# Performance work log

Measured on AMD Instinct MI355X. Metric: run time of the kernel, lower is better.

## Reference

```python
import jax, jax.numpy as jnp
import numpy as np

L = 2        # n_layers
IN = 172     # in_channels
HID = 128    # hidden_channels
NH = 4       # heads
HD = HID // NH  # per-head dim = 32
TD = 100     # time_dim
V = 400000   # global node table size
N = 150000   # sampled subgraph nodes
E = 500000   # edges per layer
B = 15000    # seed batch size


def setup_inputs() -> dict:
    key = jax.random.key(0)
    ks = jax.random.split(key, 24)
    p = lambda k, shp, s=0.05: jax.random.normal(k, shp, jnp.float32) * s
    inp = {
        "x_all": jax.random.normal(ks[0], (V, IN), jnp.float32),
        "all_node_ids": jax.random.randint(ks[1], (N,), 0, V),
        "edge_src": jax.random.randint(ks[2], (L, E), 0, N),
        "edge_dst": jax.random.randint(ks[3], (L, E), 0, N),
        "dts": jax.random.uniform(ks[4], (L, E), jnp.float32, 0.0, 1e4),
        "batch_size": B,
        # TimeEncode params
        "basis_freq": jnp.asarray(1.0 / 10 ** np.linspace(0, 9, TD), jnp.float32),
        "phase": jnp.zeros((TD,), jnp.float32),
        # input projection
        "Wp": p(ks[5], (IN, HID)), "bp": jnp.zeros((HID,), jnp.float32),
        # per-layer TransformerConv params (stacked over L)
        "Wq": p(ks[6], (L, HID, HID)), "bq": jnp.zeros((L, HID), jnp.float32),
        "Wk": p(ks[7], (L, HID, HID)), "bk": jnp.zeros((L, HID), jnp.float32),
        "Wv": p(ks[8], (L, HID, HID)), "bv": jnp.zeros((L, HID), jnp.float32),
        "We": p(ks[9], (L, TD, HID)),  # lin_edge, bias=False in PyG
        "Wskip": p(ks[10], (L, HID, HID)), "bskip": jnp.zeros((L, HID), jnp.float32),
        "bn_g": jnp.ones((L, HID), jnp.float32), "bn_b": jnp.zeros((L, HID), jnp.float32),
        # classifier head
        "W1": p(ks[11], (HID, HID)), "b1": jnp.zeros((HID,), jnp.float32),
        "g1": jnp.ones((HID,), jnp.float32), "be1": jnp.zeros((HID,), jnp.float32),
        "W2": p(ks[12], (HID, HID // 2)), "b2": jnp.zeros((HID // 2,), jnp.float32),
        "g2": jnp.ones((HID // 2,), jnp.float32), "be2": jnp.zeros((HID // 2,), jnp.float32),
        "W3": p(ks[13], (HID // 2, 1)), "b3": jnp.zeros((1,), jnp.float32),
    }
    return inp


def _bn(x, g, b):
    # BatchNorm1d, training-mode batch statistics (biased variance), eps=1e-5
    m = x.mean(0)
    v = x.var(0)
    return g * (x - m) * jax.lax.rsqrt(v + 1e-5) + b


def reference(x_all, all_node_ids, edge_src, edge_dst, dts, batch_size,
              basis_freq, phase, Wp, bp, Wq, bq, Wk, bk, Wv, bv, We,
              Wskip, bskip, bn_g, bn_b, W1, b1, g1, be1, W2, b2, g2, be2, W3, b3):
    n = all_node_ids.shape[0]
    x = x_all[all_node_ids]                      # [N, IN] gather from global table
    h = jax.nn.relu(x @ Wp + bp)                 # [N, HID]
    inv_sqrt_d = 1.0 / np.sqrt(HD)
    for i in range(L):
        src, dst, dt = edge_src[i], edge_dst[i], dts[i]
        # learnable sinusoidal time encoding of edge delta-t  [E, TD]
        te = jnp.cos(dt[:, None] * basis_freq[None, :] + phase[None, :])
        q = (h @ Wq[i] + bq[i]).reshape(n, NH, HD)
        k = (h @ Wk[i] + bk[i]).reshape(n, NH, HD)
        v = (h @ Wv[i] + bv[i]).reshape(n, NH, HD)
        e = (te @ We[i]).reshape(-1, NH, HD)     # [E, NH, HD]
        kj = k[src] + e                          # key + edge proj (PyG TransformerConv)
        vj = v[src] + e                          # value + edge proj
        alpha = jnp.einsum('ehd,ehd->eh', q[dst], kj) * inv_sqrt_d  # [E, NH]
        # scatter-softmax over edges grouped by destination node
        m = jax.ops.segment_max(alpha, dst, num_segments=n)
        a = jnp.exp(alpha - m[dst])
        s = jax.ops.segment_sum(a, dst, num_segments=n) + 1e-16
        w = a / s[dst]                           # [E, NH]
        agg = jax.ops.segment_sum(w[:, :, None] * vj, dst, num_segments=n)
        out = agg.reshape(n, HID) + h @ Wskip[i] + bskip[i]  # concat heads + root skip
        h = _bn(jax.nn.relu(out), bn_g[i], bn_b[i])          # dropout = identity (eval)
    hb = h[:batch_size]
    z = jax.nn.relu(_bn(hb @ W1 + b1, g1, be1))
    z = jax.nn.relu(_bn(z @ W2 + b2, g2, be2))
    return (z @ W3 + b3)[:, 0]                   # [batch_size]
```

## Files before the change

kernel.cpp:

```cpp
#include <hip/hip_runtime.h>
#include <hip/hip_bf16.h>
#include <math.h>

#define IN_DIM 172
#define HID 128
#define TDIM 100
#define KPAD 192

typedef __attribute__((ext_vector_type(8))) short bf16x8;
typedef __attribute__((ext_vector_type(4))) float f32x4;

static __device__ __forceinline__ ushort f2b(float x) {
  unsigned u = __float_as_uint(x);
  u += 0x7FFFu + ((u >> 16) & 1u);
  return (ushort)(u >> 16);
}
static __device__ __forceinline__ float blo(unsigned w) { return __uint_as_float(w << 16); }
static __device__ __forceinline__ float bhi(unsigned w) { return __uint_as_float(w & 0xffff0000u); }
static __device__ __forceinline__ float b2f(ushort v) { return __uint_as_float((unsigned)v << 16); }

__global__ void k_prep(const float* __restrict__ Wp,
                       const float* __restrict__ Wq, const float* __restrict__ Wk,
                       const float* __restrict__ Wv, const float* __restrict__ Ws,
                       const float* __restrict__ bq, const float* __restrict__ bk,
                       const float* __restrict__ bv, const float* __restrict__ bs,
                       const float* __restrict__ We, const float* __restrict__ W1,
                       ushort* __restrict__ wpt,
                       ushort* __restrict__ wallT0, ushort* __restrict__ wallT1,
                       float* __restrict__ ball0, float* __restrict__ ball1,
                       ushort* __restrict__ wet0, ushort* __restrict__ wet1,
                       ushort* __restrict__ w1t) {
  int i = blockIdx.x * 256 + threadIdx.x;
  if (i < 128 * KPAD) {
    int c = i / KPAD, k = i - c * KPAD;
    wpt[i] = (k < IN_DIM) ? f2b(Wp[k * HID + c]) : (ushort)0;
    return;
  }
  i -= 128 * KPAD;
  if (i < 2 * 512 * 128) {
    int layer = i >> 16;
    int j = i & 65535;
    int col = j >> 7, k = j & 127;
    int m = col >> 7, c = col & 127;
    const float* W = (m == 0) ? Wq : (m == 1) ? Wk : (m == 2) ? Wv : Ws;
    W += (size_t)layer * HID * HID;
    (layer ? wallT1 : wallT0)[j] = f2b(W[k * HID + c]);
    if (k == 0) {
      const float* bb = (m == 0) ? bq : (m == 1) ? bk : (m == 2) ? bv : bs;
      (layer ? ball1 : ball0)[col] = bb[layer * HID + c];
    }
    return;
  }
  i -= 2 * 512 * 128;
  if (i < 2 * 128 * 128) {
    int layer = i >> 14;
    int j = i & 16383;
    int c = j >> 7, t = j & 127;
    (layer ? wet1 : wet0)[j] =
        (t < TDIM) ? f2b(We[((size_t)layer * TDIM + t) * HID + c]) : (ushort)0;
    return;
  }
  i -= 2 * 128 * 128;
  if (i < 128 * 128) {
    int c = i >> 7, k = i & 127;
    w1t[i] = f2b(W1[k * HID + c]);
  }
}

__global__ __launch_bounds__(256) void k_in_mfma(
    const float* __restrict__ x_all, const int* __restrict__ ids,
    const ushort* __restrict__ wpt, const float* __restrict__ bp,
    ushort* __restrict__ h, int n) {
  __shared__ __align__(16) ushort xs[64][200];
  int tid = threadIdx.x;
  long r0 = (long)blockIdx.x * 64;
  for (int i = tid; i < 64 * 28; i += 256) {
    int r = i / 28, c = IN_DIM + (i - r * 28);
    xs[r][c] = 0;
  }
  for (int i = tid; i < 64 * 43; i += 256) {
    int r = i / 43, seg = i - r * 43;
    long row = r0 + r;
    float4 v = make_float4(0.f, 0.f, 0.f, 0.f);
    if (row < n) v = *(const float4*)(x_all + (size_t)ids[row] * IN_DIM + seg * 4);
    ushort4 u;
    u.x = f2b(v.x); u.y = f2b(v.y); u.z = f2b(v.z); u.w = f2b(v.w);
    *(ushort4*)&xs[r][seg * 4] = u;
  }
  __syncthreads();
  int wv = tid >> 6, l = tid & 63;
  int arow = wv * 16 + (l & 15);
  int kb0 = (l >> 4) * 8;
  bf16x8 a[6];
  #pragma unroll
  for (int kk = 0; kk < 6; ++kk) a[kk] = *(const bf16x8*)&xs[arow][kk * 32 + kb0];
  #pragma unroll
  for (int nt = 0; nt < 8; ++nt) {
    int col = nt * 16 + (l & 15);
    const ushort* wcol = wpt + (size_t)col * KPAD + kb0;
    f32x4 acc = {0.f, 0.f, 0.f, 0.f};
    #pragma unroll
    for (int kk = 0; kk < 6; ++kk) {
      bf16x8 bfr = *(const bf16x8*)(wcol + kk * 32);
      acc = __builtin_amdgcn_mfma_f32_16x16x32_bf16(a[kk], bfr, acc, 0, 0, 0);
    }
    float bias = bp[col];
    #pragma unroll
    for (int j = 0; j < 4; ++j) {
      long row = r0 + wv * 16 + (l >> 4) * 4 + j;
      if (row < n) {
        float y = acc[j] + bias;
        h[row * HID + col] = f2b(y > 0.f ? y : 0.f);
      }
    }
  }
}

template <bool BN_IN>
__global__ __launch_bounds__(512) void k_qkvs(
    const ushort* __restrict__ hbf, const ushort* __restrict__ xf,
    const float* __restrict__ sums, const float* __restrict__ bng,
    const float* __restrict__ bnb, float inv_n,
    const ushort* __restrict__ wallT, const float* __restrict__ ball,
    ushort* __restrict__ qb, ushort* __restrict__ kvb,
    ushort* __restrict__ ob, int n) {
  __shared__ __align__(16) ushort hs[128][136];
  __shared__ float As[128], Bs[128];
  int tid = threadIdx.x;
  if (BN_IN) {
    if (tid < 128) {
      float mean = sums[tid] * inv_n;
      float var = sums[128 + tid] * inv_n - mean * mean;
      float A = bng[tid] * rsqrtf(var + 1e-5f);
      As[tid] = A;
      Bs[tid] = bnb[tid] - mean * A;
    }
    __syncthreads();
  }
  long r0 = (long)blockIdx.x * 128;
  for (int i = tid; i < 128 * 16; i += 512) {
    int r = i >> 4, cseg = i & 15;
    long row = r0 + r;
    int c0 = cseg * 8;
    if (BN_IN) {
      ushort4 ua = {0, 0, 0, 0}, ub = {0, 0, 0, 0};
      if (row < n) {
        uint4 xw = *(const uint4*)(xf + row * HID + c0);
        float x0 = blo(xw.x), x1 = bhi(xw.x), x2 = blo(xw.y), x3 = bhi(xw.y);
        float x4 = blo(xw.z), x5 = bhi(xw.z), x6 = blo(xw.w), x7 = bhi(xw.w);
        ua.x = f2b(As[c0 + 0] * fmaxf(x0, 0.f) + Bs[c0 + 0]);
        ua.y = f2b(As[c0 + 1] * fmaxf(x1, 0.f) + Bs[c0 + 1]);
        ua.z = f2b(As[c0 + 2] * fmaxf(x2, 0.f) + Bs[c0 + 2]);
        ua.w = f2b(As[c0 + 3] * fmaxf(x3, 0.f) + Bs[c0 + 3]);
        ub.x = f2b(As[c0 + 4] * fmaxf(x4, 0.f) + Bs[c0 + 4]);
        ub.y = f2b(As[c0 + 5] * fmaxf(x5, 0.f) + Bs[c0 + 5]);
        ub.z = f2b(As[c0 + 6] * fmaxf(x6, 0.f) + Bs[c0 + 6]);
        ub.w = f2b(As[c0 + 7] * fmaxf(x7, 0.f) + Bs[c0 + 7]);
      }
      *(ushort4*)&hs[r][c0] = ua;
      *(ushort4*)&hs[r][c0 + 4] = ub;
    } else {
      bf16x8 zv = {0, 0, 0, 0, 0, 0, 0, 0};
      bf16x8 v = (row < n) ? *(const bf16x8*)&hbf[row * HID + c0] : zv;
      *(bf16x8*)&hs[r][c0] = v;
    }
  }
  int wv = tid >> 6, l = tid & 63;
  int kb0 = (l >> 4) * 8;
  int Cw = wv * 64;
  int m = wv >> 1;
  bf16x8 b[4][4];
  float bias4[4];
  #pragma unroll
  for (int ct = 0; ct < 4; ++ct) {
    int col = Cw + ct * 16 + (l & 15);
    bias4[ct] = ball[col];
    #pragma unroll
    for (int kk = 0; kk < 4; ++kk)
      b[ct][kk] = *(const bf16x8*)&wallT[(size_t)col * 128 + kk * 32 + kb0];
  }
  __syncthreads();
  #pragma unroll 2
  for (int rt = 0; rt < 8; ++rt) {
    bf16x8 a[4];
    #pragma unroll
    for (int kk = 0; kk < 4; ++kk)
      a[kk] = *(const bf16x8*)&hs[rt * 16 + (l & 15)][kk * 32 + kb0];
    f32x4 acc[4];
    #pragma unroll
    for (int ct = 0; ct < 4; ++ct) acc[ct] = (f32x4){0.f, 0.f, 0.f, 0.f};
    #pragma unroll
    for (int kk = 0; kk < 4; ++kk) {
      #pragma unroll
      for (int ct = 0; ct < 4; ++ct)
        acc[ct] = __builtin_amdgcn_mfma_f32_16x16x32_bf16(a[kk], b[ct][kk], acc[ct], 0, 0, 0);
    }
    #pragma unroll
    for (int ct = 0; ct < 4; ++ct) {
      int cc = (wv & 1) * 64 + ct * 16 + (l & 15);
      #pragma unroll
      for (int j = 0; j < 4; ++j) {
        long row = r0 + rt * 16 + (l >> 4) * 4 + j;
        if (row < n) {
          float y = acc[ct][j] + bias4[ct];
          if (m == 0) qb[row * HID + cc] = f2b(y);
          else if (m == 1) kvb[row * 256 + cc] = f2b(y);
          else if (m == 2) kvb[row * 256 + 128 + cc] = f2b(y);
          else ob[row * HID + cc] = f2b(y);
        }
      }
    }
  }
}

__global__ __launch_bounds__(256) void k_mfma128_bn(
    const ushort* __restrict__ xf, const float* __restrict__ sums,
    const float* __restrict__ bng, const float* __restrict__ bnb, float inv_n,
    const ushort* __restrict__ WT, const float* __restrict__ bias,
    float* __restrict__ Y, float* __restrict__ zsums, int n) {
  __shared__ __align__(16) ushort hs[64][136];
  __shared__ float As[128], Bs[128];
  __shared__ float zs1[128], zs2[128];
  int tid = threadIdx.x;
  if (tid < 128) {
    float mean = sums[tid] * inv_n;
    float var = sums[128 + tid] * inv_n - mean * mean;
    float A = bng[tid] * rsqrtf(var + 1e-5f);
    As[tid] = A;
    Bs[tid] = bnb[tid] - mean * A;
    zs1[tid] = 0.f;
    zs2[tid] = 0.f;
  }
  __syncthreads();
  long r0 = (long)blockIdx.x * 64;
  for (int i = tid; i < 64 * 16; i += 256) {
    int r = i >> 4, cseg = i & 15;
    long row = r0 + r;
    int c0 = cseg * 8;
    ushort4 ua = {0, 0, 0, 0}, ub = {0, 0, 0, 0};
    if (row < n) {
      uint4 xw = *(const uint4*)(xf + row * HID + c0);
      float x0 = blo(xw.x), x1 = bhi(xw.x), x2 = blo(xw.y), x3 = bhi(xw.y);
      float x4 = blo(xw.z), x5 = bhi(xw.z), x6 = blo(xw.w), x7 = bhi(xw.w);
      ua.x = f2b(As[c0 + 0] * fmaxf(x0, 0.f) + Bs[c0 + 0]);
      ua.y = f2b(As[c0 + 1] * fmaxf(x1, 0.f) + Bs[c0 + 1]);
      ua.z = f2b(As[c0 + 2] * fmaxf(x2, 0.f) + Bs[c0 + 2]);
      ua.w = f2b(As[c0 + 3] * fmaxf(x3, 0.f) + Bs[c0 + 3]);
      ub.x = f2b(As[c0 + 4] * fmaxf(x4, 0.f) + Bs[c0 + 4]);
      ub.y = f2b(As[c0 + 5] * fmaxf(x5, 0.f) + Bs[c0 + 5]);
      ub.z = f2b(As[c0 + 6] * fmaxf(x6, 0.f) + Bs[c0 + 6]);
      ub.w = f2b(As[c0 + 7] * fmaxf(x7, 0.f) + Bs[c0 + 7]);
    }
    *(ushort4*)&hs[r][c0] = ua;
    *(ushort4*)&hs[r][c0 + 4] = ub;
  }
  __syncthreads();
  int wv = tid >> 6, l = tid & 63;
  int arow = wv * 16 + (l & 15);
  int kb0 = (l >> 4) * 8;
  bf16x8 a[4];
  #pragma unroll
  for (int kk = 0; kk < 4; ++kk) a[kk] = *(const bf16x8*)&hs[arow][kk * 32 + kb0];
  #pragma unroll
  for (int nt = 0; nt < 8; ++nt) {
    int col = nt * 16 + (l & 15);
    const ushort* wcol = WT + (size_t)col * 128 + kb0;
    f32x4 acc = {0.f, 0.f, 0.f, 0.f};
    #pragma unroll
    for (int kk = 0; kk < 4; ++kk) {
      bf16x8 bfr = *(const bf16x8*)(wcol + kk * 32);
      acc = __builtin_amdgcn_mfma_f32_16x16x32_bf16(a[kk], bfr, acc, 0, 0, 0);
    }
    float bs = bias[col];
    float ts = 0.f, tss = 0.f;
    #pragma unroll
    for (int j = 0; j < 4; ++j) {
      long row = r0 + wv * 16 + (l >> 4) * 4 + j;
      if (row < n) {
        float y = acc[j] + bs;
        Y[row * HID + col] = y;
        ts += y;
        tss += y * y;
      }
    }
    atomicAdd(&zs1[col], ts);
    atomicAdd(&zs2[col], tss);
  }
  __syncthreads();
  if (tid < 128) {
    atomicAdd(&zsums[tid], zs1[tid]);
    atomicAdd(&zsums[128 + tid], zs2[tid]);
  }
}

__global__ void k_hist2(const int* __restrict__ dst_all, int* __restrict__ counts,
                        int n, int nE2, int nE) {
  int e = blockIdx.x * 256 + threadIdx.x;
  if (e >= nE2) return;
  int layer = (e >= nE) ? 1 : 0;
  atomicAdd(&counts[layer * n + dst_all[e]], 1);
}

__global__ void k_scan_chunk(const int* __restrict__ counts, int* __restrict__ offs,
                             int* __restrict__ chunkSums, int m) {
  __shared__ int ls[256];
  int t = threadIdx.x;
  int base = blockIdx.x * 1024 + t * 4;
  int v[4];
  #pragma unroll
  for (int j = 0; j < 4; ++j) v[j] = (base + j < m) ? counts[base + j] : 0;
  ls[t] = v[0] + v[1] + v[2] + v[3];
  __syncthreads();
  for (int off = 1; off < 256; off <<= 1) {
    int x = (t >= off) ? ls[t - off] : 0;
    __syncthreads();
    ls[t] += x;
    __syncthreads();
  }
  int run = (t == 0) ? 0 : ls[t - 1];
  if (t == 255) chunkSums[blockIdx.x] = ls[255];
  #pragma unroll
  for (int j = 0; j < 4; ++j) {
    if (base + j < m) offs[base + j] = run;
    run += v[j];
  }
}

__global__ __launch_bounds__(512) void k_scan_tops(int* __restrict__ chunkSums, int nchunks) {
  __shared__ int ls[512];
  int t = threadIdx.x;
  ls[t] = (t < nchunks) ? chunkSums[t] : 0;
  __syncthreads();
  for (int off = 1; off < 512; off <<= 1) {
    int x = (t >= off) ? ls[t - off] : 0;
    __syncthreads();
    ls[t] += x;
    __syncthreads();
  }
  int excl = (t == 0) ? 0 : ls[t - 1];
  if (t < nchunks) chunkSums[t] = excl;
}

__global__ void k_scan_add(int* __restrict__ offs, const int* __restrict__ chunkSums,
                           int m, int totalE) {
  int i = blockIdx.x * 256 + threadIdx.x;
  if (i < m) offs[i] += chunkSums[i >> 10];
  if (i == 0) offs[m] = totalE;
}

__global__ void k_scatter2(const int* __restrict__ src_all, const int* __restrict__ dst_all,
                           const float* __restrict__ dts_all, const int* __restrict__ offs,
                           int* __restrict__ cursor, uint2* __restrict__ edata,
                           int n, int nE2, int nE) {
  int e = blockIdx.x * 256 + threadIdx.x;
  if (e >= nE2) return;
  int layer = (e >= nE) ? 1 : 0;
  int d = layer * n + dst_all[e];
  int pos = offs[d] + atomicAdd(&cursor[d], 1);
  edata[pos] = make_uint2((unsigned)src_all[e], __float_as_uint(dts_all[e]));
}

__global__ __launch_bounds__(256) void k_te_mfma(
    const uint2* __restrict__ edata, const float* __restrict__ freq,
    const float* __restrict__ phase, const ushort* __restrict__ wet,
    ushort* __restrict__ eb, int nE) {
  __shared__ __align__(16) ushort te[64][136];
  __shared__ float dt_s[64];
  __shared__ float fr_s[128], ph_s[128];
  int tid = threadIdx.x;
  if (tid < 128) {
    fr_s[tid] = (tid < TDIM) ? freq[tid] : 0.f;
    ph_s[tid] = (tid < TDIM) ? phase[tid] : 0.f;
  }
  long e0 = (long)blockIdx.x << 6;
  if (tid < 64) dt_s[tid] = (e0 + tid < nE) ? __uint_as_float(edata[e0 + tid].y) : 0.f;
  __syncthreads();
  for (int i = tid; i < 64 * 128; i += 256) {
    int el = i >> 7, t = i & 127;
    float val = (t < TDIM) ? __cosf(dt_s[el] * fr_s[t] + ph_s[t]) : 0.f;
    te[el][t] = f2b(val);
  }
  __syncthreads();
  int wv = tid >> 6, l = tid & 63;
  int arow = wv * 16 + (l & 15);
  int kb0 = (l >> 4) * 8;
  bf16x8 a[4];
  #pragma unroll
  for (int kk = 0; kk < 4; ++kk) a[kk] = *(const bf16x8*)&te[arow][kk * 32 + kb0];
  __syncthreads();
  #pragma unroll
  for (int nt = 0; nt < 8; ++nt) {
    int col = nt * 16 + (l & 15);
    const ushort* wcol = wet + (size_t)col * 128 + kb0;
    f32x4 acc = {0.f, 0.f, 0.f, 0.f};
    #pragma unroll
    for (int kk = 0; kk < 4; ++kk) {
      bf16x8 bfr = *(const bf16x8*)(wcol + kk * 32);
      acc = __builtin_amdgcn_mfma_f32_16x16x32_bf16(a[kk], bfr, acc, 0, 0, 0);
    }
    #pragma unroll
    for (int j = 0; j < 4; ++j)
      te[wv * 16 + (l >> 4) * 4 + j][col] = f2b(acc[j]);
  }
  __syncthreads();
  for (int i = tid; i < 64 * 16; i += 256) {
    int r = i >> 4, cs = i & 15;
    long row = e0 + r;
    if (row < nE) *(bf16x8*)&eb[row * 128 + cs * 8] = *(const bf16x8*)&te[r][cs * 8];
  }
}

__global__ void k_attn(const int* __restrict__ offs_l, const uint2* __restrict__ edata,
                       int bias, const ushort* __restrict__ eb,
                       const ushort* __restrict__ qb, const ushort* __restrict__ kvb,
                       ushort* __restrict__ ob, int n) {
  int d = (blockIdx.x * 256 + threadIdx.x) >> 4;
  if (d >= n) return;
  int cl = threadIdx.x & 15;
  int c0 = cl * 8;
  int beg = offs_l[d], end = offs_l[d + 1];
  if (beg == end) return;
  const ushort* ebl = eb - (size_t)bias * HID;
  uint4 qw = *(const uint4*)(qb + (size_t)d * HID + c0);
  float q0 = blo(qw.x), q1 = bhi(qw.x), q2 = blo(qw.y), q3 = bhi(qw.y);
  float q4 = blo(qw.z), q5 = bhi(qw.z), q6 = blo(qw.w), q7 = bhi(qw.w);
  float s = 0.f;
  float a0 = 0.f, a1 = 0.f, a2 = 0.f, a3 = 0.f, a4 = 0.f, a5 = 0.f, a6 = 0.f, a7 = 0.f;
  for (int pos = beg; pos < end; ++pos) {
    int sv = (int)edata[pos].x;
    uint4 kw = *(const uint4*)(kvb + (size_t)sv * 256 + c0);
    uint4 vw = *(const uint4*)(kvb + (size_t)sv * 256 + 128 + c0);
    uint4 ew = *(const uint4*)(ebl + (size_t)pos * HID + c0);
    float e0 = blo(ew.x), e1 = bhi(ew.x), e2 = blo(ew.y), e3 = bhi(ew.y);
    float e4 = blo(ew.z), e5 = bhi(ew.z), e6 = blo(ew.w), e7 = bhi(ew.w);
    float p = q0 * (blo(kw.x) + e0) + q1 * (bhi(kw.x) + e1) +
              q2 * (blo(kw.y) + e2) + q3 * (bhi(kw.y) + e3) +
              q4 * (blo(kw.z) + e4) + q5 * (bhi(kw.z) + e5) +
              q6 * (blo(kw.w) + e6) + q7 * (bhi(kw.w) + e7);
    p += __shfl_xor(p, 1);
    p += __shfl_xor(p, 2);
    float pe = __expf(p * 0.17677669529663687f);
    s += pe;
    a0 += pe * (blo(vw.x) + e0);
    a1 += pe * (bhi(vw.x) + e1);
    a2 += pe * (blo(vw.y) + e2);
    a3 += pe * (bhi(vw.y) + e3);
    a4 += pe * (blo(vw.z) + e4);
    a5 += pe * (bhi(vw.z) + e5);
    a6 += pe * (blo(vw.w) + e6);
    a7 += pe * (bhi(vw.w) + e7);
  }
  float inv = 1.f / (s + 1e-16f);
  uint4* o = (uint4*)(ob + (size_t)d * HID + c0);
  uint4 ow = *o;
  float y0 = blo(ow.x) + a0 * inv, y1 = bhi(ow.x) + a1 * inv;
  float y2 = blo(ow.y) + a2 * inv, y3 = bhi(ow.y) + a3 * inv;
  float y4 = blo(ow.z) + a4 * inv, y5 = bhi(ow.z) + a5 * inv;
  float y6 = blo(ow.w) + a6 * inv, y7 = bhi(ow.w) + a7 * inv;
  uint4 w;
  w.x = (unsigned)f2b(y0) | ((unsigned)f2b(y1) << 16);
  w.y = (unsigned)f2b(y2) | ((unsigned)f2b(y3) << 16);
  w.z = (unsigned)f2b(y4) | ((unsigned)f2b(y5) << 16);
  w.w = (unsigned)f2b(y6) | ((unsigned)f2b(y7) << 16);
  *o = w;
}

__global__ void k_bn_reduce_b(const ushort* __restrict__ X, int n,
                              float* __restrict__ sums) {
  int col = threadIdx.x & 127;
  int rloc = threadIdx.x >> 7;
  float s = 0.f, s2 = 0.f;
  for (long r = (long)blockIdx.x * 2 + rloc; r < n; r += (long)gridDim.x * 2) {
    float v = b2f(X[r * HID + col]);
    v = v > 0.f ? v : 0.f;
    s += v; s2 += v * v;
  }
  __shared__ float ls[256], ls2[256];
  ls[threadIdx.x] = s; ls2[threadIdx.x] = s2;
  __syncthreads();
  if (rloc == 0) {
    s += ls[128 + col]; s2 += ls2[128 + col];
    atomicAdd(&sums[col], s);
    atomicAdd(&sums[128 + col], s2);
  }
}

__global__ __launch_bounds__(256) void k_gemm_64(
    const float* __restrict__ X, const float* __restrict__ sums,
    const float* __restrict__ g, const float* __restrict__ be, float inv_n,
    const float* __restrict__ W, const float* __restrict__ b,
    float* __restrict__ Y, float* __restrict__ zsums, int n) {
  __shared__ float xs[16][HID];
  __shared__ float As[128], Bs[128];
  __shared__ float zs1[64], zs2[64];
  if (threadIdx.x < 128) {
    int c = threadIdx.x;
    float mean = sums[c] * inv_n;
    float var = sums[128 + c] * inv_n - mean * mean;
    float A = g[c] * rsqrtf(var + 1e-5f);
    As[c] = A;
    Bs[c] = be[c] - mean * A;
    if (c < 64) { zs1[c] = 0.f; zs2[c] = 0.f; }
  }
  __syncthreads();
  int r0 = blockIdx.x * 16;
  for (int idx = threadIdx.x; idx < 16 * HID; idx += 256) {
    int r = idx >> 7, c = idx & 127;
    int row = r0 + r;
    float v = (row < n) ? X[(size_t)row * HID + c] : 0.f;
    v = As[c] * v + Bs[c];
    xs[r][c] = v > 0.f ? v : 0.f;
  }
  __syncthreads();
  int col = threadIdx.x & 63;
  int rg = threadIdx.x >> 6;
  float acc[4] = {0.f, 0.f, 0.f, 0.f};
  #pragma unroll 4
  for (int kk = 0; kk < HID; ++kk) {
    float w = W[kk * 64 + col];
    #pragma unroll
    for (int j = 0; j < 4; ++j) acc[j] += xs[rg + 4 * j][kk] * w;
  }
  float bias = b[col];
  float ts = 0.f, tss = 0.f;
  #pragma unroll
  for (int j = 0; j < 4; ++j) {
    int row = r0 + rg + 4 * j;
    if (row < n) {
      float y = acc[j] + bias;
      Y[(size_t)row * 64 + col] = y;
      ts += y;
      tss += y * y;
    }
  }
  atomicAdd(&zs1[col], ts);
  atomicAdd(&zs2[col], tss);
  __syncthreads();
  if (threadIdx.x < 64) {
    atomicAdd(&zsums[threadIdx.x], zs1[threadIdx.x]);
    atomicAdd(&zsums[64 + threadIdx.x], zs2[threadIdx.x]);
  }
}

__global__ __launch_bounds__(256) void k_final(
    const float* __restrict__ z2, const float* __restrict__ sums,
    const float* __restrict__ g2, const float* __restrict__ be2, float inv_n,
    const float* __restrict__ W3, const float* __restrict__ b3,
    float* __restrict__ out, int n) {
  int wave = threadIdx.x >> 6, lane = threadIdx.x & 63;
  int row = blockIdx.x * 4 + wave;
  if (row >= n) return;
  float z = z2[(size_t)row * 64 + lane];
  float mean = sums[lane] * inv_n;
  float var = sums[64 + lane] * inv_n - mean * mean;
  float v = g2[lane] * (z - mean) * rsqrtf(var + 1e-5f) + be2[lane];
  v = v > 0.f ? v : 0.f;
  float pv = v * W3[lane];
  pv += __shfl_xor(pv, 1);
  pv += __shfl_xor(pv, 2);
  pv += __shfl_xor(pv, 4);
  pv += __shfl_xor(pv, 8);
  pv += __shfl_xor(pv, 16);
  pv += __shfl_xor(pv, 32);
  if (lane == 0) out[row] = pv + b3[0];
}

extern "C" void kernel_launch(void* const* d_in, const int* in_sizes, int n_in,
                              void* d_out, int out_size, void* d_ws, size_t ws_size,
                              hipStream_t stream) {
  const float* x_all = (const float*)d_in[0];
  const int* ids = (const int*)d_in[1];
  const int* esrc = (const int*)d_in[2];
  const int* edst = (const int*)d_in[3];
  const float* dts = (const float*)d_in[4];
  const float* freq = (const float*)d_in[6];
  const float* phase = (const float*)d_in[7];
  const float* Wp = (const float*)d_in[8];
  const float* bp = (const float*)d_in[9];
  const float* Wq = (const float*)d_in[10];
  const float* bq = (const float*)d_in[11];
  const float* Wk = (const float*)d_in[12];
  const float* bk = (const float*)d_in[13];
  const float* Wv = (const float*)d_in[14];
  const float* bv = (const float*)d_in[15];
  const float* We = (const float*)d_in[16];
  const float* Wskip = (const float*)d_in[17];
  const float* bskip = (const float*)d_in[18];
  const float* bn_g = (const float*)d_in[19];
  const float* bn_b = (const float*)d_in[20];
  const float* W1 = (const float*)d_in[21];
  const float* b1 = (const float*)d_in[22];
  const float* g1 = (const float*)d_in[23];
  const float* be1 = (const float*)d_in[24];
  const float* W2 = (const float*)d_in[25];
  const float* b2 = (const float*)d_in[26];
  const float* g2 = (const float*)d_in[27];
  const float* be2 = (const float*)d_in[28];
  const float* W3 = (const float*)d_in[29];
  const float* b3 = (const float*)d_in[30];

  size_t n = (size_t)in_sizes[1];
  size_t nE = (size_t)in_sizes[2] / 2;
  size_t nE2 = nE * 2;
  int B = out_size;

  char* pc = (char*)d_ws;
  auto alloc = [&](size_t bytes) { char* r = pc; pc += (bytes + 255) & ~(size_t)255; return r; };
  ushort* h    = (ushort*)alloc(n * HID * 2);
  ushort* qb   = (ushort*)alloc(n * HID * 2);
  ushort* kvb  = (ushort*)alloc(n * 256 * 2);
  ushort* ob0  = (ushort*)alloc(n * HID * 2);
  ushort* ob1  = (ushort*)alloc(n * HID * 2);
  ushort* eb0  = (ushort*)alloc(nE * HID * 2);
  ushort* eb1  = (ushort*)alloc(nE * HID * 2);
  uint2* edata = (uint2*)alloc(nE2 * 8);
  int* offs    = (int*)alloc((2 * n + 2) * 4);
  int* chunkS  = (int*)alloc(512 * 4);
  size_t zbytes = 4 * n * 4 + 4 * 256 * 4;
  char* zb = alloc(zbytes);
  int* counts = (int*)zb;
  int* cursor = counts + 2 * n;
  float* sumsL0 = (float*)(cursor + 2 * n);
  float* sumsL1 = sumsL0 + 256;
  float* sumsZ1 = sumsL1 + 256;
  float* sumsZ2 = sumsZ1 + 256;
  ushort* wpt    = (ushort*)alloc(128 * KPAD * 2);
  ushort* wallT0 = (ushort*)alloc(512 * 128 * 2);
  ushort* wallT1 = (ushort*)alloc(512 * 128 * 2);
  float* ball0   = (float*)alloc(512 * 4);
  float* ball1   = (float*)alloc(512 * 4);
  ushort* wet0   = (ushort*)alloc(128 * 128 * 2);
  ushort* wet1   = (ushort*)alloc(128 * 128 * 2);
  ushort* w1t    = (ushort*)alloc(128 * 128 * 2);
  float* z1      = (float*)alloc((size_t)B * HID * 4);
  float* z2      = (float*)alloc((size_t)B * 64 * 4);

  int gn64 = (int)((n + 63) / 64);
  int gn128 = (int)((n + 127) / 128);
  int ge2 = (int)((nE2 + 255) / 256);
  int eblk = (int)((nE + 63) / 64);
  int m2 = (int)(2 * n);
  int nchunks = (m2 + 1023) / 1024;
  float inv_nf = 1.f / (float)n;
  float inv_bf = 1.f / (float)B;

  hipMemsetAsync(zb, 0, zbytes, stream);
  k_prep<<<(128 * KPAD + 2 * 512 * 128 + 2 * 128 * 128 + 128 * 128 + 255) / 256, 256, 0, stream>>>(
      Wp, Wq, Wk, Wv, Wskip, bq, bk, bv, bskip, We, W1,
      wpt, wallT0, wallT1, ball0, ball1, wet0, wet1, w1t);

  k_hist2<<<ge2, 256, 0, stream>>>(edst, counts, (int)n, (int)nE2, (int)nE);
  k_scan_chunk<<<nchunks, 256, 0, stream>>>(counts, offs, chunkS, m2);
  k_scan_tops<<<1, 512, 0, stream>>>(chunkS, nchunks);
  k_scan_add<<<(m2 + 255) / 256, 256, 0, stream>>>(offs, chunkS, m2, (int)nE2);
  k_scatter2<<<ge2, 256, 0, stream>>>(esrc, edst, dts, offs, cursor, edata,
                                      (int)n, (int)nE2, (int)nE);

  k_te_mfma<<<eblk, 256, 0, stream>>>(edata, freq, phase, wet0, eb0, (int)nE);

  k_in_mfma<<<gn64, 256, 0, stream>>>(x_all, ids, wpt, bp, h, (int)n);

  for (int i = 0; i < 2; ++i) {
    const ushort* wallT = i ? wallT1 : wallT0;
    const float* ball = i ? ball1 : ball0;
    const ushort* eb = i ? eb1 : eb0;
    ushort* ob = i ? ob1 : ob0;
    int bias = i * (int)nE;

    if (i == 1)
      k_te_mfma<<<eblk, 256, 0, stream>>>(edata + nE, freq, phase, wet1, eb1, (int)nE);

    if (i == 0)
      k_qkvs<false><<<gn128, 512, 0, stream>>>(h, nullptr, nullptr, nullptr, nullptr, 0.f,
                                               wallT, ball, qb, kvb, ob, (int)n);
    else
      k_qkvs<true><<<gn128, 512, 0, stream>>>(nullptr, ob0, sumsL0, bn_g, bn_b, inv_nf,
                                              wallT, ball, qb, kvb, ob, (int)n);

    k_attn<<<(int)((n + 15) / 16), 256, 0, stream>>>(offs + (size_t)i * n, edata, bias,
                                                     eb, qb, kvb, ob, (int)n);
    k_bn_reduce_b<<<512, 256, 0, stream>>>(ob, (int)n, i ? sumsL1 : sumsL0);
  }

  k_mfma128_bn<<<(B + 63) / 64, 256, 0, stream>>>(ob1, sumsL1, bn_g + HID, bn_b + HID,
                                                  inv_nf, w1t, b1, z1, sumsZ1, B);
  k_gemm_64<<<(B + 15) / 16, 256, 0, stream>>>(z1, sumsZ1, g1, be1, inv_bf, W2, b2,
                                               z2, sumsZ2, B);
  k_final<<<(B + 3) / 4, 256, 0, stream>>>(z2, sumsZ2, g2, be2, inv_bf, W3, b3,
                                           (float*)d_out, B);
}
```

Before: 967.2 us.

## Fuse BatchNorm statistic reduction into attention kernel and unroll edge loop by two

The attention kernel now accumulates per-column ReLU sums and sums of squares of its bf16 output in shared memory, then flushes them to global with atomics. This removes the separate BN-reduce pass that re-read the whole node output buffer. The edge loop is also unrolled by two so that two edges' K/V/E gathers are in flight at once. The cost is many shared-memory atomics per thread (16 per thread, contended across the 16 nodes in a block), one global atomic flush per block across about 9.4k blocks, and higher register pressure from the unroll.

```diff
diff --git a/kernel.cpp b/kernel.cpp
--- a/kernel.cpp
+++ b/kernel.cpp
@@ -410,78 +410,123 @@
   }
 }
 
-__global__ void k_attn(const int* __restrict__ offs_l, const uint2* __restrict__ edata,
-                       int bias, const ushort* __restrict__ eb,
-                       const ushort* __restrict__ qb, const ushort* __restrict__ kvb,
-                       ushort* __restrict__ ob, int n) {
-  int d = (blockIdx.x * 256 + threadIdx.x) >> 4;
-  if (d >= n) return;
-  int cl = threadIdx.x & 15;
+__global__ __launch_bounds__(256) void k_attn(
+    const int* __restrict__ offs_l, const uint2* __restrict__ edata,
+    int bias, const ushort* __restrict__ eb,
+    const ushort* __restrict__ qb, const ushort* __restrict__ kvb,
+    ushort* __restrict__ ob, float* __restrict__ sums, int n) {
+  __shared__ float zs1[128], zs2[128];
+  int tid = threadIdx.x;
+  if (tid < 128) { zs1[tid] = 0.f; zs2[tid] = 0.f; }
+  __syncthreads();
+  int d = (blockIdx.x * 256 + tid) >> 4;
+  int cl = tid & 15;
   int c0 = cl * 8;
-  int beg = offs_l[d], end = offs_l[d + 1];
-  if (beg == end) return;
-  const ushort* ebl = eb - (size_t)bias * HID;
-  uint4 qw = *(const uint4*)(qb + (size_t)d * HID + c0);
-  float q0 = blo(qw.x), q1 = bhi(qw.x), q2 = blo(qw.y), q3 = bhi(qw.y);
-  float q4 = blo(qw.z), q5 = bhi(qw.z), q6 = blo(qw.w), q7 = bhi(qw.w);
-  float s = 0.f;
-  float a0 = 0.f, a1 = 0.f, a2 = 0.f, a3 = 0.f, a4 = 0.f, a5 = 0.f, a6 = 0.f, a7 = 0.f;
-  for (int pos = beg; pos < end; ++pos) {
-    int sv = (int)edata[pos].x;
-    uint4 kw = *(const uint4*)(kvb + (size_t)sv * 256 + c0);
-    uint4 vw = *(const uint4*)(kvb + (size_t)sv * 256 + 128 + c0);
-    uint4 ew = *(const uint4*)(ebl + (size_t)pos * HID + c0);
-    float e0 = blo(ew.x), e1 = bhi(ew.x), e2 = blo(ew.y), e3 = bhi(ew.y);
-    float e4 = blo(ew.z), e5 = bhi(ew.z), e6 = blo(ew.w), e7 = bhi(ew.w);
-    float p = q0 * (blo(kw.x) + e0) + q1 * (bhi(kw.x) + e1) +
-              q2 * (blo(kw.y) + e2) + q3 * (bhi(kw.y) + e3) +
-              q4 * (blo(kw.z) + e4) + q5 * (bhi(kw.z) + e5) +
-              q6 * (blo(kw.w) + e6) + q7 * (bhi(kw.w) + e7);
-    p += __shfl_xor(p, 1);
-    p += __shfl_xor(p, 2);
-    float pe = __expf(p * 0.17677669529663687f);
-    s += pe;
-    a0 += pe * (blo(vw.x) + e0);
-    a1 += pe * (bhi(vw.x) + e1);
-    a2 += pe * (blo(vw.y) + e2);
-    a3 += pe * (bhi(vw.y) + e3);
-    a4 += pe * (blo(vw.z) + e4);
-    a5 += pe * (bhi(vw.z) + e5);
-    a6 += pe * (blo(vw.w) + e6);
-    a7 += pe * (bhi(vw.w) + e7);
-  }
-  float inv = 1.f / (s + 1e-16f);
-  uint4* o = (uint4*)(ob + (size_t)d * HID + c0);
-  uint4 ow = *o;
-  float y0 = blo(ow.x) + a0 * inv, y1 = bhi(ow.x) + a1 * inv;
-  float y2 = blo(ow.y) + a2 * inv, y3 = bhi(ow.y) + a3 * inv;
-  float y4 = blo(ow.z) + a4 * inv, y5 = bhi(ow.z) + a5 * inv;
-  float y6 = blo(ow.w) + a6 * inv, y7 = bhi(ow.w) + a7 * inv;
-  uint4 w;
-  w.x = (unsigned)f2b(y0) | ((unsigned)f2b(y1) << 16);
-  w.y = (unsigned)f2b(y2) | ((unsigned)f2b(y3) << 16);
-  w.z = (unsigned)f2b(y4) | ((unsigned)f2b(y5) << 16);
-  w.w = (unsigned)f2b(y6) | ((unsigned)f2b(y7) << 16);
-  *o = w;
-}
-
-__global__ void k_bn_reduce_b(const ushort* __restrict__ X, int n,
-                              float* __restrict__ sums) {
-  int col = threadIdx.x & 127;
-  int rloc = threadIdx.x >> 7;
-  float s = 0.f, s2 = 0.f;
-  for (long r = (long)blockIdx.x * 2 + rloc; r < n; r += (long)gridDim.x * 2) {
-    float v = b2f(X[r * HID + col]);
-    v = v > 0.f ? v : 0.f;
-    s += v; s2 += v * v;
-  }
-  __shared__ float ls[256], ls2[256];
-  ls[threadIdx.x] = s; ls2[threadIdx.x] = s2;
-  __syncthreads();
-  if (rloc == 0) {
-    s += ls[128 + col]; s2 += ls2[128 + col];
-    atomicAdd(&sums[col], s);
-    atomicAdd(&sums[128 + col], s2);
+  bool active = d < n;
+  float y0 = 0.f, y1 = 0.f, y2 = 0.f, y3 = 0.f, y4 = 0.f, y5 = 0.f, y6 = 0.f, y7 = 0.f;
+  if (active) {
+    int beg = offs_l[d], end = offs_l[d + 1];
+    uint4 ow = *(const uint4*)(ob + (size_t)d * HID + c0);
+    y0 = blo(ow.x); y1 = bhi(ow.x); y2 = blo(ow.y); y3 = bhi(ow.y);
+    y4 = blo(ow.z); y5 = bhi(ow.z); y6 = blo(ow.w); y7 = bhi(ow.w);
+    if (beg < end) {
+      const ushort* ebl = eb - (size_t)bias * HID;
+      uint4 qw = *(const uint4*)(qb + (size_t)d * HID + c0);
+      float q0 = blo(qw.x), q1 = bhi(qw.x), q2 = blo(qw.y), q3 = bhi(qw.y);
+      float q4 = blo(qw.z), q5 = bhi(qw.z), q6 = blo(qw.w), q7 = bhi(qw.w);
+      float s = 0.f;
+      float a0 = 0.f, a1 = 0.f, a2 = 0.f, a3 = 0.f;
+      float a4 = 0.f, a5 = 0.f, a6 = 0.f, a7 = 0.f;
+      int pos = beg;
+      for (; pos + 2 <= end; pos += 2) {
+        int svA = (int)edata[pos].x;
+        int svB = (int)edata[pos + 1].x;
+        uint4 kwA = *(const uint4*)(kvb + (size_t)svA * 256 + c0);
+        uint4 vwA = *(const uint4*)(kvb + (size_t)svA * 256 + 128 + c0);
+        uint4 ewA = *(const uint4*)(ebl + (size_t)pos * HID + c0);
+        uint4 kwB = *(const uint4*)(kvb + (size_t)svB * 256 + c0);
+        uint4 vwB = *(const uint4*)(kvb + (size_t)svB * 256 + 128 + c0);
+        uint4 ewB = *(const uint4*)(ebl + (size_t)(pos + 1) * HID + c0);
+        float eA0 = blo(ewA.x), eA1 = bhi(ewA.x), eA2 = blo(ewA.y), eA3 = bhi(ewA.y);
+        float eA4 = blo(ewA.z), eA5 = bhi(ewA.z), eA6 = blo(ewA.w), eA7 = bhi(ewA.w);
+        float eB0 = blo(ewB.x), eB1 = bhi(ewB.x), eB2 = blo(ewB.y), eB3 = bhi(ewB.y);
+        float eB4 = blo(ewB.z), eB5 = bhi(ewB.z), eB6 = blo(ewB.w), eB7 = bhi(ewB.w);
+        float pA = q0 * (blo(kwA.x) + eA0) + q1 * (bhi(kwA.x) + eA1) +
+                   q2 * (blo(kwA.y) + eA2) + q3 * (bhi(kwA.y) + eA3) +
+                   q4 * (blo(kwA.z) + eA4) + q5 * (bhi(kwA.z) + eA5) +
+                   q6 * (blo(kwA.w) + eA6) + q7 * (bhi(kwA.w) + eA7);
+        float pB = q0 * (blo(kwB.x) + eB0) + q1 * (bhi(kwB.x) + eB1) +
+                   q2 * (blo(kwB.y) + eB2) + q3 * (bhi(kwB.y) + eB3) +
+                   q4 * (blo(kwB.z) + eB4) + q5 * (bhi(kwB.z) + eB5) +
+                   q6 * (blo(kwB.w) + eB6) + q7 * (bhi(kwB.w) + eB7);
+        pA += __shfl_xor(pA, 1);
+        pA += __shfl_xor(pA, 2);
+        pB += __shfl_xor(pB, 1);
+        pB += __shfl_xor(pB, 2);
+        float peA = __expf(pA * 0.17677669529663687f);
+        float peB = __expf(pB * 0.17677669529663687f);
+        s += peA + peB;
+        a0 += peA * (blo(vwA.x) + eA0) + peB * (blo(vwB.x) + eB0);
+        a1 += peA * (bhi(vwA.x) + eA1) + peB * (bhi(vwB.x) + eB1);
+        a2 += peA * (blo(vwA.y) + eA2) + peB * (blo(vwB.y) + eB2);
+        a3 += peA * (bhi(vwA.y) + eA3) + peB * (bhi(vwB.y) + eB3);
+        a4 += peA * (blo(vwA.z) + eA4) + peB * (blo(vwB.z) + eB4);
+        a5 += peA * (bhi(vwA.z) + eA5) + peB * (bhi(vwB.z) + eB5);
+        a6 += peA * (blo(vwA.w) + eA6) + peB * (blo(vwB.w) + eB6);
+        a7 += peA * (bhi(vwA.w) + eA7) + peB * (bhi(vwB.w) + eB7);
+      }
+      if (pos < end) {
+        int sv = (int)edata[pos].x;
+        uint4 kw = *(const uint4*)(kvb + (size_t)sv * 256 + c0);
+        uint4 vw = *(const uint4*)(kvb + (size_t)sv * 256 + 128 + c0);
+        uint4 ew = *(const uint4*)(ebl + (size_t)pos * HID + c0);
+        float e0 = blo(ew.x), e1 = bhi(ew.x), e2 = blo(ew.y), e3 = bhi(ew.y);
+        float e4 = blo(ew.z), e5 = bhi(ew.z), e6 = blo(ew.w), e7 = bhi(ew.w);
+        float p = q0 * (blo(kw.x) + e0) + q1 * (bhi(kw.x) + e1) +
+                  q2 * (blo(kw.y) + e2) + q3 * (bhi(kw.y) + e3) +
+                  q4 * (blo(kw.z) + e4) + q5 * (bhi(kw.z) + e5) +
+                  q6 * (blo(kw.w) + e6) + q7 * (bhi(kw.w) + e7);
+        p += __shfl_xor(p, 1);
+        p += __shfl_xor(p, 2);
+        float pe = __expf(p * 0.17677669529663687f);
+        s += pe;
+        a0 += pe * (blo(vw.x) + e0);
+        a1 += pe * (bhi(vw.x) + e1);
+        a2 += pe * (blo(vw.y) + e2);
+        a3 += pe * (bhi(vw.y) + e3);
+        a4 += pe * (blo(vw.z) + e4);
+        a5 += pe * (bhi(vw.z) + e5);
+        a6 += pe * (blo(vw.w) + e6);
+        a7 += pe * (bhi(vw.w) + e7);
+      }
+      float inv = 1.f / (s + 1e-16f);
+      y0 += a0 * inv; y1 += a1 * inv; y2 += a2 * inv; y3 += a3 * inv;
+      y4 += a4 * inv; y5 += a5 * inv; y6 += a6 * inv; y7 += a7 * inv;
+      ushort u0 = f2b(y0), u1 = f2b(y1), u2 = f2b(y2), u3 = f2b(y3);
+      ushort u4 = f2b(y4), u5 = f2b(y5), u6 = f2b(y6), u7 = f2b(y7);
+      uint4 w;
+      w.x = (unsigned)u0 | ((unsigned)u1 << 16);
+      w.y = (unsigned)u2 | ((unsigned)u3 << 16);
+      w.z = (unsigned)u4 | ((unsigned)u5 << 16);
+      w.w = (unsigned)u6 | ((unsigned)u7 << 16);
+      *(uint4*)(ob + (size_t)d * HID + c0) = w;
+      y0 = b2f(u0); y1 = b2f(u1); y2 = b2f(u2); y3 = b2f(u3);
+      y4 = b2f(u4); y5 = b2f(u5); y6 = b2f(u6); y7 = b2f(u7);
+    }
+    float r;
+    r = fmaxf(y0, 0.f); atomicAdd(&zs1[c0 + 0], r); atomicAdd(&zs2[c0 + 0], r * r);
+    r = fmaxf(y1, 0.f); atomicAdd(&zs1[c0 + 1], r); atomicAdd(&zs2[c0 + 1], r * r);
+    r = fmaxf(y2, 0.f); atomicAdd(&zs1[c0 + 2], r); atomicAdd(&zs2[c0 + 2], r * r);
+    r = fmaxf(y3, 0.f); atomicAdd(&zs1[c0 + 3], r); atomicAdd(&zs2[c0 + 3], r * r);
+    r = fmaxf(y4, 0.f); atomicAdd(&zs1[c0 + 4], r); atomicAdd(&zs2[c0 + 4], r * r);
+    r = fmaxf(y5, 0.f); atomicAdd(&zs1[c0 + 5], r); atomicAdd(&zs2[c0 + 5], r * r);
+    r = fmaxf(y6, 0.f); atomicAdd(&zs1[c0 + 6], r); atomicAdd(&zs2[c0 + 6], r * r);
+    r = fmaxf(y7, 0.f); atomicAdd(&zs1[c0 + 7], r); atomicAdd(&zs2[c0 + 7], r * r);
+  }
+  __syncthreads();
+  if (tid < 128) {
+    atomicAdd(&sums[tid], zs1[tid]);
+    atomicAdd(&sums[128 + tid], zs2[tid]);
   }
 }
 
@@ -678,8 +723,8 @@
                                               wallT, ball, qb, kvb, ob, (int)n);
 
     k_attn<<<(int)((n + 15) / 16), 256, 0, stream>>>(offs + (size_t)i * n, edata, bias,
-                                                     eb, qb, kvb, ob, (int)n);
-    k_bn_reduce_b<<<512, 256, 0, stream>>>(ob, (int)n, i ? sumsL1 : sumsL0);
+                                                     eb, qb, kvb, ob,
+                                                     i ? sumsL1 : sumsL0, (int)n);
   }
 
   k_mfma128_bn<<<(B + 63) / 64, 256, 0, stream>>>(ob1, sumsL1, bn_g + HID, bn_b + HID,
```

Measured after the change: 1.276 ms. 1.32x slower.
